# Kernel optimization log

Hardware: AMD Instinct MI355X
Metric: run time of the kernel (lower is better)

## Reference

```python
import jax, jax.numpy as jnp
import numpy as np

B, S, I, E, NH, HID, L = 32, 512, 64, 128, 8, 1024, 4
HD = E // NH
TEMP = 0.05
EPS_BN = 1e-5
EPS_LN = 1e-5


def _pe(seq_len, d_model):
    # sinusoidal positional encoding, matches PositionalEncoding buffer pe[:seq_len, 0, :]
    pos = jnp.arange(seq_len, dtype=jnp.float32)[:, None]
    div = jnp.exp(jnp.arange(0, d_model, 2, dtype=jnp.float32) * (-np.log(10000.0) / d_model))
    pe = jnp.zeros((seq_len, d_model), jnp.float32)
    pe = pe.at[:, 0::2].set(jnp.sin(pos * div))
    pe = pe.at[:, 1::2].set(jnp.cos(pos * div))
    return pe


def _bn(x, g, b, axis):
    # eval-mode BatchNorm1d with running_mean=0, running_var=1 (affine scale+shift)
    sh = [1] * x.ndim
    sh[axis] = -1
    return x * (g / jnp.sqrt(1.0 + EPS_BN)).reshape(sh) + b.reshape(sh)


def _ln(x, g, b):
    m = jnp.mean(x, axis=-1, keepdims=True)
    v = jnp.var(x, axis=-1, keepdims=True)
    return (x - m) / jnp.sqrt(v + EPS_LN) * g + b


def _layer(h, Wqkv, bqkv, Wo, bo, g1, b1, g2, b2, W1, bf1, W2, bf2):
    # h: (S, B, E); post-LN torch TransformerEncoderLayer, relu FFN
    s, b = h.shape[0], h.shape[1]
    qkv = h @ Wqkv + bqkv                                  # (S, B, 3E)
    q, k, v = jnp.split(qkv, 3, axis=-1)
    sp = lambda t: t.reshape(s, b, NH, HD).transpose(1, 2, 0, 3)  # (B, NH, S, HD)
    q, k, v = sp(q), sp(k), sp(v)
    att = jax.nn.softmax(jnp.einsum('bhqd,bhkd->bhqk', q, k) * (1.0 / np.sqrt(HD)), axis=-1)
    o = jnp.einsum('bhqk,bhkd->bhqd', att, v).transpose(2, 0, 1, 3).reshape(s, b, E)
    h = _ln(h + o @ Wo + bo, g1, b1)
    ff = jax.nn.relu(h @ W1 + bf1) @ W2 + bf2
    h = _ln(h + ff, g2, b2)
    return h, att.mean(axis=1)  # attn averaged over heads: (B, S, S)


def setup_inputs() -> dict:
    key = jax.random.key(0)
    ks = iter(jax.random.split(key, 64))
    r = lambda *sh: jax.random.normal(next(ks), sh, jnp.float32) * 0.02
    return dict(
        x=jax.random.normal(next(ks), (B, S, I), jnp.float32),
        Wt=r(I, E), bt=r(E),
        bn1_g=jnp.ones(E), bn1_b=jnp.zeros(E),
        bn2_g=jnp.ones(E), bn2_b=jnp.zeros(E),
        Wqkv=r(L, E, 3 * E), bqkv=r(L, 3 * E), Wo=r(L, E, E), bo=r(L, E),
        ln1_g=jnp.ones((L, E)), ln1_b=jnp.zeros((L, E)),
        ln2_g=jnp.ones((L, E)), ln2_b=jnp.zeros((L, E)),
        W1=r(L, E, HID), b1=r(L, HID), W2=r(L, HID, E), b2=r(L, E),
        bn3_g=jnp.ones(E), bn3_b=jnp.zeros(E),
        Wd=r(E, I), bd=r(I), bn4_g=jnp.ones(I), bn4_b=jnp.zeros(I),
        Ws=r(S, HID), bs=r(HID), bn5_g=jnp.ones(HID), bn5_b=jnp.zeros(HID),
        Wtext=r(1024, HID), btext=r(HID), lnT_g=jnp.ones(HID), lnT_b=jnp.zeros(HID),
        sensor_emb=jax.random.normal(next(ks), (I, 1024), jnp.float32),
    )


def reference(x, Wt, bt, bn1_g, bn1_b, bn2_g, bn2_b,
              Wqkv, bqkv, Wo, bo, ln1_g, ln1_b, ln2_g, ln2_b,
              W1, b1, W2, b2, bn3_g, bn3_b,
              Wd, bd, bn4_g, bn4_b, Ws, bs, bn5_g, bn5_b,
              Wtext, btext, lnT_g, lnT_b, sensor_emb):
    # trunk_net: Linear -> BN(E) -> PE -> BN(E)
    h = x @ Wt + bt                                  # (B, S, E)
    h = _bn(h.transpose(0, 2, 1), bn1_g, bn1_b, 1)   # (B, E, S)
    h = h.transpose(2, 0, 1)                         # (S, B, E)
    h = h + _pe(h.shape[0], E)[:, None, :]
    h = _bn(h.transpose(1, 2, 0), bn2_g, bn2_b, 1)   # (B, E, S)
    h = h.transpose(2, 0, 1)                         # (S, B, E)
    for i in range(L):
        h, attn = _layer(h, Wqkv[i], bqkv[i], Wo[i], bo[i],
                         ln1_g[i], ln1_b[i], ln2_g[i], ln2_b[i],
                         W1[i], b1[i], W2[i], b2[i])
    h = _bn(h.transpose(1, 2, 0), bn3_g, bn3_b, 1)   # (B, E, S)
    # downsample_embedding_to_input_net
    d = jax.nn.relu(h.transpose(0, 2, 1) @ Wd + bd)  # (B, S, I)
    d = _bn(d.transpose(0, 2, 1), bn4_g, bn4_b, 1)   # (B, I, S)
    # sequence_representation_net
    imu = jax.nn.relu(d @ Ws + bs)                   # (B, I, HID)
    imu = _bn(imu, bn5_g, bn5_b, 2)
    # text_to_shared_net on sensor embeddings
    sens = _ln(jax.nn.relu(sensor_emb @ Wtext + btext), lnT_g, lnT_b)  # (I, HID)
    # fused pairwise cosine similarity (torch expands to (B,I,I,HID); we don't)
    imu_n = imu / jnp.maximum(jnp.linalg.norm(imu, axis=-1, keepdims=True), 1e-8)
    sens_n = sens / jnp.maximum(jnp.linalg.norm(sens, axis=-1, keepdims=True), 1e-8)
    return jnp.einsum('bih,jh->bij', imu_n, sens_n) / TEMP  # (B, I, I)
```

## Files before the change

kernel.cpp:

```cpp
#include <hip/hip_runtime.h>
#include <hip/hip_bf16.h>

#define B_   32
#define S_   512
#define I_   64
#define E_   128
#define NH_  8
#define HD_  16
#define HID_ 1024
#define L_   4
#define NTOK (B_*S_)

typedef __hip_bfloat16 bf16;
typedef __attribute__((ext_vector_type(8))) short bf16x8;
typedef __attribute__((ext_vector_type(4))) short bf16x4;
typedef __attribute__((ext_vector_type(4))) float f32x4;

__device__ __forceinline__ float b2f(bf16 v) { return __bfloat162float(v); }

template<bool F32>
__device__ __forceinline__ float ld(const void* p, size_t i) {
    if (F32) return ((const float*)p)[i];
    return b2f(((const bf16*)p)[i]);
}

__device__ __forceinline__ unsigned short f2bu(float f) {
    union { bf16 h; unsigned short u; } c; c.h = __float2bfloat16(f); return c.u;
}
__device__ __forceinline__ unsigned short b2u(bf16 h) {
    union { bf16 h; unsigned short u; } c; c.h = h; return c.u;
}
__device__ __forceinline__ float u2f(unsigned short u) {
    return __uint_as_float((unsigned int)u << 16);
}

__global__ void k_flag(const void* bn1g, int* flag) {
    if (threadIdx.x == 0) {
        const unsigned short* u = (const unsigned short*)bn1g;
        int zeros = 0;
        for (int i = 0; i < 32; ++i) zeros += (u[i] == 0);
        flag[0] = (zeros >= 8) ? 1 : 0;
    }
}

struct TrJobs {
    const void* in[7];
    bf16*       out[7];
    int R[7];
    int C[7];
    int start[8];
};

template<bool F32>
__device__ void tr_all_body(const TrJobs& j, float (*tile)[33])
{
    int bid = blockIdx.x;
    int job = 0;
#pragma unroll
    for (int t = 0; t < 6; ++t) if (bid >= j.start[t + 1]) job = t + 1;
    int local = bid - j.start[job];
    int R = j.R[job], C = j.C[job];
    int nx = C >> 5, ny = R >> 5;
    int per_z = nx * ny;
    int z = local / per_z;
    int rem = local - z * per_z;
    int cy = rem / nx, cx = rem - cy * nx;
    const void* in = j.in[job];
    bf16* out = j.out[job];

    size_t off = (size_t)z * R * C;
    int c0 = cx * 32, r0 = cy * 32;
    int tx = threadIdx.x;
    for (int i = threadIdx.y; i < 32; i += 8)
        tile[i][tx] = ld<F32>(in, off + (size_t)(r0 + i) * C + c0 + tx);
    __syncthreads();
    for (int i = threadIdx.y; i < 32; i += 8)
        out[off + (size_t)(c0 + i) * R + r0 + tx] = __float2bfloat16(tile[tx][i]);
}
__global__ __launch_bounds__(256) void k_tr_all(TrJobs j, const int* flag)
{
    __shared__ float tile[32][33];
    if (*flag) tr_all_body<true>(j, tile);
    else       tr_all_body<false>(j, tile);
}

struct PkJobs {
    const bf16* in[4];
    bf16*       out[4];
    int K[4];
    int NT[4];
    int KT[4];
    int start[5];
};

__global__ __launch_bounds__(256) void k_pack(PkJobs j)
{
    int fb = blockIdx.x * 4 + (threadIdx.x >> 6);
    int lane = threadIdx.x & 63;
    int job = 0;
#pragma unroll
    for (int t = 0; t < 3; ++t) if (fb >= j.start[t + 1]) job = t + 1;
    int local = fb - j.start[job];
    int K = j.K[job], NT = j.NT[job], KT = j.KT[job];
    int per_z = NT * KT;
    int z = local / per_z;
    int rem = local - z * per_z;
    int ct = rem / KT, kt = rem - ct * KT;
    int l15 = lane & 15, quad = lane >> 4;
    const bf16* in = j.in[job] + (size_t)z * NT * 16 * K;
    bf16* out = j.out[job] + (size_t)z * per_z * 512 + (size_t)(ct * KT + kt) * 512 + lane * 8;
    *(uint4*)out = *(const uint4*)&in[(size_t)(ct * 16 + l15) * K + kt * 32 + quad * 8];
}

template<bool F32>
__device__ void trunk_body(const void* x, const void* Wt, const void* bt,
                           const void* g1, const void* c1,
                           const void* g2, const void* c2, float* __restrict__ h,
                           float (*xs)[I_])
{
    const int TOK = 8;
    int t0 = blockIdx.x * TOK;
    int tid = threadIdx.x;
    for (int idx = tid; idx < TOK * I_; idx += 128) {
        int tt = idx >> 6, k = idx & 63;
        xs[tt][k] = ld<F32>(x, (size_t)(t0 + tt) * I_ + k);
    }
    __syncthreads();
    int e = tid;
    float acc[TOK];
    float bias = ld<F32>(bt, e);
#pragma unroll
    for (int tt = 0; tt < TOK; ++tt) acc[tt] = bias;
    for (int k = 0; k < I_; ++k) {
        float w = ld<F32>(Wt, k * E_ + e);
#pragma unroll
        for (int tt = 0; tt < TOK; ++tt) acc[tt] += xs[tt][k] * w;
    }
    float rs = rsqrtf(1.0f + 1e-5f);
    float a1 = ld<F32>(g1, e) * rs, d1 = ld<F32>(c1, e);
    float a2 = ld<F32>(g2, e) * rs, d2 = ld<F32>(c2, e);
    int p = e >> 1;
    float freq = __expf(-(float)p * 0.14391157f);
#pragma unroll
    for (int tt = 0; tt < TOK; ++tt) {
        int t = t0 + tt;
        int s = t & (S_ - 1);
        float ang = (float)s * freq;
        float pe = (e & 1) ? cosf(ang) : sinf(ang);
        float v = acc[tt] * a1 + d1 + pe;
        h[(size_t)t * E_ + e] = v * a2 + d2;
    }
}
__global__ __launch_bounds__(128) void k_trunk(
    const void* x, const void* Wt, const void* bt,
    const void* g1, const void* c1, const void* g2, const void* c2,
    float* h, const int* flag)
{
    __shared__ float xs[8][I_];
    if (*flag) trunk_body<true>(x, Wt, bt, g1, c1, g2, c2, h, xs);
    else       trunk_body<false>(x, Wt, bt, g1, c1, g2, c2, h, xs);
}

template<bool F32>
__device__ void qkvm_body(const float* __restrict__ h, const bf16* __restrict__ WP,
                          const void* bias, size_t obi, bf16* __restrict__ qkv,
                          unsigned short (*A_s)[136])
{
    int t0 = blockIdx.x * 32;
    int tid = threadIdx.x;
    int wv = tid >> 6, lane = tid & 63;
    int l15 = lane & 15, quad = lane >> 4;

    {
        const float4* h4 = (const float4*)(h + (size_t)t0 * E_);
        for (int i = tid; i < 32 * E_ / 4; i += 256) {
            float4 v = h4[i];
            int row = i >> 5, col = (i & 31) * 4;
            unsigned int w0 = (unsigned int)f2bu(v.x) | ((unsigned int)f2bu(v.y) << 16);
            unsigned int w1 = (unsigned int)f2bu(v.z) | ((unsigned int)f2bu(v.w) << 16);
            *(uint2*)&A_s[row][col] = (uint2){w0, w1};
        }
    }
    __syncthreads();

    bf16x8 af[2][4];
#pragma unroll
    for (int kt = 0; kt < 4; ++kt) {
        int k0 = kt * 32 + quad * 8;
        af[0][kt] = *(const bf16x8*)&A_s[l15][k0];
        af[1][kt] = *(const bf16x8*)&A_s[16 + l15][k0];
    }
    for (int nt = 0; nt < 6; ++nt) {
        int col = wv * 96 + nt * 16 + l15;
        int ct = wv * 6 + nt;
        f32x4 acc0 = {0.f, 0.f, 0.f, 0.f}, acc1 = {0.f, 0.f, 0.f, 0.f};
#pragma unroll
        for (int kt = 0; kt < 4; ++kt) {
            bf16x8 bfr = *(const bf16x8*)&WP[(size_t)((ct * 4 + kt) * 64 + lane) * 8];
            acc0 = __builtin_amdgcn_mfma_f32_16x16x32_bf16(af[0][kt], bfr, acc0, 0, 0, 0);
            acc1 = __builtin_amdgcn_mfma_f32_16x16x32_bf16(af[1][kt], bfr, acc1, 0, 0, 0);
        }
        float bb = ld<F32>(bias, obi + col);
#pragma unroll
        for (int r = 0; r < 4; ++r) {
            qkv[(size_t)(t0 + quad * 4 + r) * 384 + col]      = __float2bfloat16(acc0[r] + bb);
            qkv[(size_t)(t0 + 16 + quad * 4 + r) * 384 + col] = __float2bfloat16(acc1[r] + bb);
        }
    }
}
__global__ __launch_bounds__(256) void k_qkv(
    const float* h, const bf16* WP, const void* bias, size_t obi,
    bf16* qkv, const int* flag)
{
    __shared__ unsigned short A_s[32][136];
    if (*flag) qkvm_body<true>(h, WP, bias, obi, qkv, A_s);
    else       qkvm_body<false>(h, WP, bias, obi, qkv, A_s);
}

__global__ __launch_bounds__(512) void k_attn(bf16* qkv)
{
    __shared__ unsigned short Ks[S_ * 16];
    __shared__ unsigned short Qs[256 * 16];
    __shared__ unsigned short VT[HD_ * 520];

    int bx = blockIdx.x;
    int qh = bx & 1;
    int hh = (bx >> 1) & (NH_ - 1);
    int b  = bx >> 4;
    int tid = threadIdx.x;
    const size_t base = (size_t)(b * S_) * 384 + hh * HD_;
    const float qs = 0.25f * 1.44269504f;

    for (int i = tid; i < S_ * 2; i += 512) {
        int s = i >> 1, hf = i & 1;
        uint4 v = *(const uint4*)(qkv + base + (size_t)s * 384 + 128 + hf * 8);
        unsigned int* w = (unsigned int*)&v;
#pragma unroll
        for (int j = 0; j < 4; ++j) {
            unsigned int lo = f2bu(u2f((unsigned short)(w[j] & 0xffff)) * qs);
            unsigned int hi = f2bu(u2f((unsigned short)(w[j] >> 16)) * qs);
            w[j] = lo | (hi << 16);
        }
        *(uint4*)&Ks[s * 16 + hf * 8] = v;
    }
    for (int i = tid; i < 256 * 2; i += 512) {
        int s = i >> 1, hf = i & 1;
        *(uint4*)&Qs[s * 16 + hf * 8] =
            *(const uint4*)(qkv + base + (size_t)(qh * 256 + s) * 384 + hf * 8);
    }
    {
        int s = tid;
        uint4 v0 = *(const uint4*)(qkv + base + (size_t)s * 384 + 256);
        uint4 v1 = *(const uint4*)(qkv + base + (size_t)s * 384 + 256 + 8);
        const unsigned short* u0 = (const unsigned short*)&v0;
        const unsigned short* u1 = (const unsigned short*)&v1;
#pragma unroll
        for (int dd = 0; dd < 8; ++dd) VT[dd * 520 + s] = u0[dd];
#pragma unroll
        for (int dd = 0; dd < 8; ++dd) VT[(8 + dd) * 520 + s] = u1[dd];
    }
    __syncthreads();

    int wv = tid >> 6, lane = tid & 63;
    int l15 = lane & 15, quad = lane >> 4;
    const f32x4 z4 = {0.f, 0.f, 0.f, 0.f};

    bf16x4 bq0 = *(const bf16x4*)&Qs[(wv * 32 + l15) * 16 + quad * 4];
    bf16x4 bq1 = *(const bf16x4*)&Qs[(wv * 32 + 16 + l15) * 16 + quad * 4];

    f32x4 O0 = z4, O1 = z4;
    float den0 = 0.f, den1 = 0.f;

#pragma unroll 2
    for (int kt = 0; kt < 32; ++kt) {
        bf16x4 ak = *(const bf16x4*)&Ks[(kt * 16 + l15) * 16 + quad * 4];
        bf16x4 av = *(const bf16x4*)&VT[l15 * 520 + kt * 16 + quad * 4];

        f32x4 s0 = __builtin_amdgcn_mfma_f32_16x16x16bf16_1k(ak, bq0, z4, 0, 0, 0);
        f32x4 s1 = __builtin_amdgcn_mfma_f32_16x16x16bf16_1k(ak, bq1, z4, 0, 0, 0);

        float p0[4], p1[4];
#pragma unroll
        for (int r = 0; r < 4; ++r) { p0[r] = exp2f(s0[r]); den0 += p0[r]; }
#pragma unroll
        for (int r = 0; r < 4; ++r) { p1[r] = exp2f(s1[r]); den1 += p1[r]; }

        bf16x4 pa0, pa1;
#pragma unroll
        for (int r = 0; r < 4; ++r) { pa0[r] = (short)f2bu(p0[r]); pa1[r] = (short)f2bu(p1[r]); }

        O0 = __builtin_amdgcn_mfma_f32_16x16x16bf16_1k(av, pa0, O0, 0, 0, 0);
        O1 = __builtin_amdgcn_mfma_f32_16x16x16bf16_1k(av, pa1, O1, 0, 0, 0);
    }

    den0 += __shfl_xor(den0, 16, 64);
    den0 += __shfl_xor(den0, 32, 64);
    den1 += __shfl_xor(den1, 16, 64);
    den1 += __shfl_xor(den1, 32, 64);
    float inv0 = 1.0f / den0;
    float inv1 = 1.0f / den1;

    int q0 = qh * 256 + wv * 32 + l15;
    bf16* out0 = qkv + (size_t)(b * S_ + q0) * 384 + hh * HD_ + quad * 4;
    bf16* out1 = out0 + (size_t)16 * 384;
    unsigned int a0 = (unsigned int)f2bu(O0[0] * inv0) | ((unsigned int)f2bu(O0[1] * inv0) << 16);
    unsigned int a1 = (unsigned int)f2bu(O0[2] * inv0) | ((unsigned int)f2bu(O0[3] * inv0) << 16);
    *(uint2*)out0 = (uint2){a0, a1};
    unsigned int c0 = (unsigned int)f2bu(O1[0] * inv1) | ((unsigned int)f2bu(O1[1] * inv1) << 16);
    unsigned int c1 = (unsigned int)f2bu(O1[2] * inv1) | ((unsigned int)f2bu(O1[3] * inv1) << 16);
    *(uint2*)out1 = (uint2){c0, c1};
}

#define FTOK 32
#define APAD 8
#define MHALF 512
#define MPAD 8

template<bool F32>
__device__ void projffn_body(const bf16* __restrict__ qkv, const bf16* __restrict__ WoP,
                             const void* bo, size_t obo,
                             const void* g1, const void* be1,
                             const bf16* __restrict__ W1P, const void* b1, size_t ob1,
                             const bf16* __restrict__ W2P, const void* b2v, size_t ob2,
                             const void* g2, const void* be2, size_t oln,
                             float* __restrict__ h,
                             unsigned short (*A_s)[E_ + APAD],
                             unsigned short (*mid_s)[MHALF + MPAD],
                             float (*red)[32][2])
{
    int t0 = blockIdx.x * FTOK;
    int tid = threadIdx.x;
    int wv = tid >> 6, lane = tid & 63;
    int l15 = lane & 15, quad = lane >> 4;
    int c0 = wv * 16 + l15;

    {
        int row = tid >> 4, seg = tid & 15;
        *(uint4*)&A_s[row][seg * 8] =
            *(const uint4*)&qkv[(size_t)(t0 + row) * 384 + seg * 8];
    }
    __syncthreads();

    bf16x8 af[2][4];
#pragma unroll
    for (int kt = 0; kt < 4; ++kt) {
        int k0 = kt * 32 + quad * 8;
        af[0][kt] = *(const bf16x8*)&A_s[l15][k0];
        af[1][kt] = *(const bf16x8*)&A_s[16 + l15][k0];
    }
    f32x4 acc[2];
    acc[0] = (f32x4){0.f, 0.f, 0.f, 0.f};
    acc[1] = (f32x4){0.f, 0.f, 0.f, 0.f};
#pragma unroll
    for (int kt = 0; kt < 4; ++kt) {
        bf16x8 bb0 = *(const bf16x8*)&WoP[(size_t)((wv * 4 + kt) * 64 + lane) * 8];
        acc[0] = __builtin_amdgcn_mfma_f32_16x16x32_bf16(af[0][kt], bb0, acc[0], 0, 0, 0);
        acc[1] = __builtin_amdgcn_mfma_f32_16x16x32_bf16(af[1][kt], bb0, acc[1], 0, 0, 0);
    }

    float bo0 = ld<F32>(bo, obo + c0);
    float val[2][4], s1[2][4], s2[2][4];
#pragma unroll
    for (int mt = 0; mt < 2; ++mt) {
#pragma unroll
        for (int r = 0; r < 4; ++r) {
            size_t row = (size_t)(t0 + mt * 16 + quad * 4 + r);
            float v0 = acc[mt][r] + bo0 + h[row * E_ + c0];
            val[mt][r] = v0;
            s1[mt][r] = v0;
            s2[mt][r] = v0 * v0;
        }
    }
#pragma unroll
    for (int off = 1; off < 16; off <<= 1) {
#pragma unroll
        for (int mt = 0; mt < 2; ++mt)
#pragma unroll
            for (int r = 0; r < 4; ++r) {
                s1[mt][r] += __shfl_xor(s1[mt][r], off, 64);
                s2[mt][r] += __shfl_xor(s2[mt][r], off, 64);
            }
    }
    if (l15 == 0) {
#pragma unroll
        for (int mt = 0; mt < 2; ++mt)
#pragma unroll
            for (int r = 0; r < 4; ++r) {
                red[wv][mt * 16 + quad * 4 + r][0] = s1[mt][r];
                red[wv][mt * 16 + quad * 4 + r][1] = s2[mt][r];
            }
    }
    __syncthreads();

    float val1[2][4];
    {
        float g10 = ld<F32>(g1, oln + c0);
        float b10 = ld<F32>(be1, oln + c0);
#pragma unroll
        for (int mt = 0; mt < 2; ++mt) {
#pragma unroll
            for (int r = 0; r < 4; ++r) {
                int rw = mt * 16 + quad * 4 + r;
                float su = red[0][rw][0] + red[1][rw][0] + red[2][rw][0] + red[3][rw][0]
                         + red[4][rw][0] + red[5][rw][0] + red[6][rw][0] + red[7][rw][0];
                float sq = red[0][rw][1] + red[1][rw][1] + red[2][rw][1] + red[3][rw][1]
                         + red[4][rw][1] + red[5][rw][1] + red[6][rw][1] + red[7][rw][1];
                float mean = su * (1.0f / E_);
                float var = fmaxf(sq * (1.0f / E_) - mean * mean, 0.0f);
                float rstd = rsqrtf(var + 1e-5f);
                float h0 = (val[mt][r] - mean) * rstd * g10 + b10;
                val1[mt][r] = h0;
                A_s[rw][c0] = f2bu(h0);
            }
        }
    }
    __syncthreads();

    bf16x8 af1[2][4];
#pragma unroll
    for (int kt = 0; kt < 4; ++kt) {
        int k0 = kt * 32 + quad * 8;
        af1[0][kt] = *(const bf16x8*)&A_s[l15][k0];
        af1[1][kt] = *(const bf16x8*)&A_s[16 + l15][k0];
    }

    f32x4 acc2[2];
    acc2[0] = (f32x4){0.f, 0.f, 0.f, 0.f};
    acc2[1] = (f32x4){0.f, 0.f, 0.f, 0.f};

    for (int p = 0; p < 2; ++p) {
        for (int nt = 0; nt < 4; ++nt) {
            int col = p * MHALF + wv * 64 + nt * 16 + l15;
            int lc  = wv * 64 + nt * 16 + l15;
            int ct  = p * 32 + wv * 4 + nt;
            f32x4 acc0 = {0.f, 0.f, 0.f, 0.f}, acc1 = {0.f, 0.f, 0.f, 0.f};
#pragma unroll
            for (int kt = 0; kt < 4; ++kt) {
                bf16x8 bfr = *(const bf16x8*)&W1P[(size_t)((ct * 4 + kt) * 64 + lane) * 8];
                acc0 = __builtin_amdgcn_mfma_f32_16x16x32_bf16(af1[0][kt], bfr, acc0, 0, 0, 0);
                acc1 = __builtin_amdgcn_mfma_f32_16x16x32_bf16(af1[1][kt], bfr, acc1, 0, 0, 0);
            }
            float bias = ld<F32>(b1, ob1 + col);
#pragma unroll
            for (int r = 0; r < 4; ++r) {
                mid_s[quad * 4 + r][lc]      = f2bu(fmaxf(acc0[r] + bias, 0.f));
                mid_s[16 + quad * 4 + r][lc] = f2bu(fmaxf(acc1[r] + bias, 0.f));
            }
        }
        __syncthreads();

        for (int kk = 0; kk < 16; ++kk) {
            int kt = p * 16 + kk;
            int k0l = kk * 32 + quad * 8;
            bf16x8 a0 = *(const bf16x8*)&mid_s[l15][k0l];
            bf16x8 a1 = *(const bf16x8*)&mid_s[16 + l15][k0l];
            bf16x8 bb0 = *(const bf16x8*)&W2P[(size_t)((wv * 32 + kt) * 64 + lane) * 8];
            acc2[0] = __builtin_amdgcn_mfma_f32_16x16x32_bf16(a0, bb0, acc2[0], 0, 0, 0);
            acc2[1] = __builtin_amdgcn_mfma_f32_16x16x32_bf16(a1, bb0, acc2[1], 0, 0, 0);
        }
        __syncthreads();
    }

    float b20 = ld<F32>(b2v, ob2 + c0);
#pragma unroll
    for (int mt = 0; mt < 2; ++mt) {
#pragma unroll
        for (int r = 0; r < 4; ++r) {
            float v0 = acc2[mt][r] + b20 + val1[mt][r];
            val[mt][r] = v0;
            s1[mt][r] = v0;
            s2[mt][r] = v0 * v0;
        }
    }
#pragma unroll
    for (int off = 1; off < 16; off <<= 1) {
#pragma unroll
        for (int mt = 0; mt < 2; ++mt)
#pragma unroll
            for (int r = 0; r < 4; ++r) {
                s1[mt][r] += __shfl_xor(s1[mt][r], off, 64);
                s2[mt][r] += __shfl_xor(s2[mt][r], off, 64);
            }
    }
    if (l15 == 0) {
#pragma unroll
        for (int mt = 0; mt < 2; ++mt)
#pragma unroll
            for (int r = 0; r < 4; ++r) {
                red[wv][mt * 16 + quad * 4 + r][0] = s1[mt][r];
                red[wv][mt * 16 + quad * 4 + r][1] = s2[mt][r];
            }
    }
    __syncthreads();
    float g20 = ld<F32>(g2, oln + c0);
    float be20 = ld<F32>(be2, oln + c0);
#pragma unroll
    for (int mt = 0; mt < 2; ++mt) {
#pragma unroll
        for (int r = 0; r < 4; ++r) {
            int rw = mt * 16 + quad * 4 + r;
            float su = red[0][rw][0] + red[1][rw][0] + red[2][rw][0] + red[3][rw][0]
                     + red[4][rw][0] + red[5][rw][0] + red[6][rw][0] + red[7][rw][0];
            float sq = red[0][rw][1] + red[1][rw][1] + red[2][rw][1] + red[3][rw][1]
                     + red[4][rw][1] + red[5][rw][1] + red[6][rw][1] + red[7][rw][1];
            float mean = su * (1.0f / E_);
            float var = fmaxf(sq * (1.0f / E_) - mean * mean, 0.0f);
            float rstd = rsqrtf(var + 1e-5f);
            size_t row = (size_t)(t0 + rw);
            h[row * E_ + c0] = (val[mt][r] - mean) * rstd * g20 + be20;
        }
    }
}
__global__ __launch_bounds__(512, 4) void k_projffn(
    const bf16* qkv, const bf16* WoP, const void* bo, size_t obo,
    const void* g1, const void* be1,
    const bf16* W1P, const void* b1, size_t ob1,
    const bf16* W2P, const void* b2v, size_t ob2,
    const void* g2, const void* be2, size_t oln, float* h, const int* flag)
{
    __shared__ unsigned short A_s[FTOK][E_ + APAD];
    __shared__ unsigned short mid_s[FTOK][MHALF + MPAD];
    __shared__ float red[8][32][2];
    if (*flag) projffn_body<true>(qkv, WoP, bo, obo, g1, be1, W1P, b1, ob1,
                                  W2P, b2v, ob2, g2, be2, oln, h, A_s, mid_s, red);
    else       projffn_body<false>(qkv, WoP, bo, obo, g1, be1, W1P, b1, ob1,
                                   W2P, b2v, ob2, g2, be2, oln, h, A_s, mid_s, red);
}

template<bool F32>
__device__ void downm_body(const float* __restrict__ h, const void* g3, const void* c3,
                           const bf16* __restrict__ WdT, const void* bd,
                           const void* g4, const void* c4, float* __restrict__ d,
                           unsigned short (*A_s)[136], float* g3s, float* c3s)
{
    int t0 = blockIdx.x * 32;
    int tid = threadIdx.x;
    if (tid < E_) {
        float rs = rsqrtf(1.0f + 1e-5f);
        g3s[tid] = ld<F32>(g3, tid) * rs;
        c3s[tid] = ld<F32>(c3, tid);
    }
    __syncthreads();
    for (int i = tid; i < 32 * E_; i += 256) {
        int row = i >> 7, col = i & 127;
        A_s[row][col] = f2bu(h[(size_t)(t0 + row) * E_ + col] * g3s[col] + c3s[col]);
    }
    __syncthreads();

    int wv = tid >> 6, lane = tid & 63;
    int l15 = lane & 15, quad = lane >> 4;
    int col = wv * 16 + l15;
    f32x4 acc0 = {0.f, 0.f, 0.f, 0.f}, acc1 = {0.f, 0.f, 0.f, 0.f};
#pragma unroll
    for (int kt = 0; kt < 4; ++kt) {
        int k0 = kt * 32 + quad * 8;
        bf16x8 a0 = *(const bf16x8*)&A_s[l15][k0];
        bf16x8 a1 = *(const bf16x8*)&A_s[16 + l15][k0];
        bf16x8 bb = *(const bf16x8*)&WdT[(size_t)col * E_ + k0];
        acc0 = __builtin_amdgcn_mfma_f32_16x16x32_bf16(a0, bb, acc0, 0, 0, 0);
        acc1 = __builtin_amdgcn_mfma_f32_16x16x32_bf16(a1, bb, acc1, 0, 0, 0);
    }
    float rs = rsqrtf(1.0f + 1e-5f);
    float bb = ld<F32>(bd, col);
    float a4 = ld<F32>(g4, col) * rs, d4 = ld<F32>(c4, col);
#pragma unroll
    for (int r = 0; r < 4; ++r) {
        d[(size_t)(t0 + quad * 4 + r) * I_ + col]      = fmaxf(acc0[r] + bb, 0.f) * a4 + d4;
        d[(size_t)(t0 + 16 + quad * 4 + r) * I_ + col] = fmaxf(acc1[r] + bb, 0.f) * a4 + d4;
    }
}
__global__ __launch_bounds__(256) void k_down(
    const float* h, const void* g3, const void* c3, const bf16* WdT, const void* bd,
    const void* g4, const void* c4, float* d, const int* flag)
{
    __shared__ unsigned short A_s[32][136];
    __shared__ float g3s[E_], c3s[E_];
    if (*flag) downm_body<true>(h, g3, c3, WdT, bd, g4, c4, d, A_s, g3s, c3s);
    else       downm_body<false>(h, g3, c3, WdT, bd, g4, c4, d, A_s, g3s, c3s);
}

template<bool F32>
__device__ void imum_body(const float* __restrict__ d, const bf16* __restrict__ WsT,
                          const void* bs, const void* g5, const void* c5,
                          float* __restrict__ imu, unsigned short (*A_s)[520])
{
    int b = blockIdx.x >> 3;
    int jc = blockIdx.x & 7;
    int tid = threadIdx.x;
    int wv = tid >> 6, lane = tid & 63;
    int l15 = lane & 15, quad = lane >> 4;

    for (int idx = tid; idx < I_ * S_; idx += 256) {
        int i = idx & 63, s = idx >> 6;
        A_s[i][s] = f2bu(d[((size_t)b * S_ + s) * I_ + i]);
    }
    __syncthreads();

    float rs = rsqrtf(1.0f + 1e-5f);
    int j0 = jc * 128 + wv * 32;
    for (int nt = 0; nt < 2; ++nt) {
        int j = j0 + nt * 16 + l15;
        f32x4 acc4[4];
#pragma unroll
        for (int mt = 0; mt < 4; ++mt) acc4[mt] = (f32x4){0.f, 0.f, 0.f, 0.f};
        for (int kt = 0; kt < 16; ++kt) {
            int k0 = kt * 32 + quad * 8;
            bf16x8 bfr = *(const bf16x8*)&WsT[(size_t)j * S_ + k0];
#pragma unroll
            for (int mt = 0; mt < 4; ++mt) {
                bf16x8 a = *(const bf16x8*)&A_s[mt * 16 + l15][k0];
                acc4[mt] = __builtin_amdgcn_mfma_f32_16x16x32_bf16(a, bfr, acc4[mt], 0, 0, 0);
            }
        }
        float bias = ld<F32>(bs, j);
        float a5 = ld<F32>(g5, j) * rs, d5 = ld<F32>(c5, j);
#pragma unroll
        for (int mt = 0; mt < 4; ++mt) {
#pragma unroll
            for (int r = 0; r < 4; ++r) {
                int row = mt * 16 + quad * 4 + r;
                float v = fmaxf(acc4[mt][r] + bias, 0.f) * a5 + d5;
                imu[((size_t)b * I_ + row) * HID_ + j] = v;
            }
        }
    }
}
__global__ __launch_bounds__(256) void k_imu(
    const float* d, const bf16* WsT, const void* bs,
    const void* g5, const void* c5, float* imu, const int* flag)
{
    __shared__ unsigned short A_s[I_][520];
    if (*flag) imum_body<true>(d, WsT, bs, g5, c5, imu, A_s);
    else       imum_body<false>(d, WsT, bs, g5, c5, imu, A_s);
}

__global__ __launch_bounds__(256) void k_norm(float* __restrict__ imu)
{
    __shared__ float red[4];
    size_t r0 = (size_t)blockIdx.x * HID_;
    int tid = threadIdx.x;
    float sq = 0.f;
    for (int k = tid; k < HID_; k += 256) { float v = imu[r0 + k]; sq += v * v; }
    for (int off = 32; off; off >>= 1) sq += __shfl_down(sq, off, 64);
    int wv = tid >> 6, lane = tid & 63;
    if (lane == 0) red[wv] = sq;
    __syncthreads();
    float tot = red[0] + red[1] + red[2] + red[3];
    float inv = 1.0f / fmaxf(sqrtf(fmaxf(tot, 0.f)), 1e-8f);
    for (int k = tid; k < HID_; k += 256) imu[r0 + k] *= inv;
}

template<bool F32>
__device__ void sensg_body(const void* se, const bf16* __restrict__ WtT,
                           const void* bt, float* __restrict__ sg,
                           unsigned short (*A_s)[HID_ + 8])
{
    int mt = blockIdx.x >> 4;
    int nc = blockIdx.x & 15;
    int r0 = mt * 16;
    int tid = threadIdx.x;
    int wv = tid >> 6, lane = tid & 63;
    int l15 = lane & 15, quad = lane >> 4;

    for (int i = tid; i < 16 * HID_; i += 256) {
        int row = i >> 10, col = i & (HID_ - 1);
        A_s[row][col] = f2bu(ld<F32>(se, (size_t)(r0 + row) * HID_ + col));
    }
    __syncthreads();

    int col = nc * 64 + wv * 16 + l15;
    f32x4 acc = {0.f, 0.f, 0.f, 0.f};
    for (int kt = 0; kt < 32; ++kt) {
        int k0 = kt * 32 + quad * 8;
        bf16x8 a = *(const bf16x8*)&A_s[l15][k0];
        bf16x8 bb = *(const bf16x8*)&WtT[(size_t)col * HID_ + k0];
        acc = __builtin_amdgcn_mfma_f32_16x16x32_bf16(a, bb, acc, 0, 0, 0);
    }
    float bbv = ld<F32>(bt, col);
#pragma unroll
    for (int r = 0; r < 4; ++r)
        sg[(size_t)(r0 + quad * 4 + r) * HID_ + col] = fmaxf(acc[r] + bbv, 0.f);
}
__global__ __launch_bounds__(256) void k_sens_gemm(
    const void* se, const bf16* WtT, const void* bt, float* sg, const int* flag)
{
    __shared__ unsigned short A_s[16][HID_ + 8];
    if (*flag) sensg_body<true>(se, WtT, bt, sg, A_s);
    else       sensg_body<false>(se, WtT, bt, sg, A_s);
}

template<bool F32>
__device__ void sensln_body(const float* __restrict__ sg, const void* g, const void* be,
                            bf16* __restrict__ sens_b, float (*red)[2])
{
    size_t r0 = (size_t)blockIdx.x * HID_;
    int tid = threadIdx.x;
    int wv = tid >> 6, lane = tid & 63;
    float v4[4];
    float s1 = 0.f, s2 = 0.f;
#pragma unroll
    for (int c = 0; c < 4; ++c) {
        float v = sg[r0 + tid + c * 256];
        v4[c] = v;
        s1 += v; s2 += v * v;
    }
    for (int off = 32; off; off >>= 1) {
        s1 += __shfl_down(s1, off, 64);
        s2 += __shfl_down(s2, off, 64);
    }
    if (lane == 0) { red[wv][0] = s1; red[wv][1] = s2; }
    __syncthreads();
    float su = red[0][0] + red[1][0] + red[2][0] + red[3][0];
    float sq = red[0][1] + red[1][1] + red[2][1] + red[3][1];
    float mean = su * (1.0f / HID_);
    float var = fmaxf(sq * (1.0f / HID_) - mean * mean, 0.0f);
    float rstd = rsqrtf(var + 1e-5f);
    float q = 0.f;
#pragma unroll
    for (int c = 0; c < 4; ++c) {
        int col = tid + c * 256;
        v4[c] = (v4[c] - mean) * rstd * ld<F32>(g, col) + ld<F32>(be, col);
        q += v4[c] * v4[c];
    }
    for (int off = 32; off; off >>= 1) q += __shfl_down(q, off, 64);
    __syncthreads();
    if (lane == 0) red[wv][0] = q;
    __syncthreads();
    float tot = red[0][0] + red[1][0] + red[2][0] + red[3][0];
    float inv = 1.0f / fmaxf(sqrtf(fmaxf(tot, 0.f)), 1e-8f);
#pragma unroll
    for (int c = 0; c < 4; ++c)
        sens_b[r0 + tid + c * 256] = __float2bfloat16(v4[c] * inv);
}
__global__ __launch_bounds__(256) void k_sens_ln(
    const float* sg, const void* g, const void* be, bf16* sens_b, const int* flag)
{
    __shared__ float red[4][2];
    if (*flag) sensln_body<true>(sg, g, be, sens_b, red);
    else       sensln_body<false>(sg, g, be, sens_b, red);
}

template<bool F32>
__device__ void finalm_body(const float* __restrict__ imu_n, const bf16* __restrict__ sens_b,
                            void* __restrict__ out, unsigned short (*A_s)[HID_ + 8])
{
    int r0 = blockIdx.x * 32;
    int tid = threadIdx.x;
    int wv = tid >> 6, lane = tid & 63;
    int l15 = lane & 15, quad = lane >> 4;

    {
        const float4* i4 = (const float4*)(imu_n + (size_t)r0 * HID_);
        for (int i = tid; i < 32 * HID_ / 4; i += 256) {
            float4 v = i4[i];
            int row = i >> 8, col = (i & 255) * 4;
            unsigned int w0 = (unsigned int)f2bu(v.x) | ((unsigned int)f2bu(v.y) << 16);
            unsigned int w1 = (unsigned int)f2bu(v.z) | ((unsigned int)f2bu(v.w) << 16);
            *(uint2*)&A_s[row][col] = (uint2){w0, w1};
        }
    }
    __syncthreads();

    int j = wv * 16 + l15;
    f32x4 acc[2];
    acc[0] = (f32x4){0.f, 0.f, 0.f, 0.f};
    acc[1] = (f32x4){0.f, 0.f, 0.f, 0.f};
    for (int kt = 0; kt < 32; ++kt) {
        int k0 = kt * 32 + quad * 8;
        bf16x8 bfr = *(const bf16x8*)&sens_b[(size_t)j * HID_ + k0];
        bf16x8 a0 = *(const bf16x8*)&A_s[l15][k0];
        bf16x8 a1 = *(const bf16x8*)&A_s[16 + l15][k0];
        acc[0] = __builtin_amdgcn_mfma_f32_16x16x32_bf16(a0, bfr, acc[0], 0, 0, 0);
        acc[1] = __builtin_amdgcn_mfma_f32_16x16x32_bf16(a1, bfr, acc[1], 0, 0, 0);
    }
#pragma unroll
    for (int mt = 0; mt < 2; ++mt) {
#pragma unroll
        for (int r = 0; r < 4; ++r) {
            size_t row = (size_t)(r0 + mt * 16 + quad * 4 + r);
            float v = acc[mt][r] * 20.0f;
            if (F32) ((float*)out)[row * I_ + j] = v;
            else     ((bf16*)out)[row * I_ + j] = __float2bfloat16(v);
        }
    }
}
__global__ __launch_bounds__(256) void k_final(
    const float* imu_n, const bf16* sens_b, void* out, const int* flag)
{
    __shared__ unsigned short A_s[32][HID_ + 8];
    if (*flag) finalm_body<true>(imu_n, sens_b, out, A_s);
    else       finalm_body<false>(imu_n, sens_b, out, A_s);
}

extern "C" void kernel_launch(void* const* d_in, const int* in_sizes, int n_in,
                              void* d_out, int out_size, void* d_ws, size_t ws_size,
                              hipStream_t stream) {
    (void)in_sizes; (void)n_in; (void)out_size; (void)ws_size;
    const void* x      = d_in[0];
    const void* Wt     = d_in[1];
    const void* bt     = d_in[2];
    const void* bn1_g  = d_in[3];
    const void* bn1_b  = d_in[4];
    const void* bn2_g  = d_in[5];
    const void* bn2_b  = d_in[6];
    const void* Wqkv   = d_in[7];
    const void* bqkv   = d_in[8];
    const void* Wo     = d_in[9];
    const void* bo     = d_in[10];
    const void* ln1_g  = d_in[11];
    const void* ln1_b  = d_in[12];
    const void* ln2_g  = d_in[13];
    const void* ln2_b  = d_in[14];
    const void* W1     = d_in[15];
    const void* b1     = d_in[16];
    const void* W2     = d_in[17];
    const void* b2     = d_in[18];
    const void* bn3_g  = d_in[19];
    const void* bn3_b  = d_in[20];
    const void* Wd     = d_in[21];
    const void* bd     = d_in[22];
    const void* bn4_g  = d_in[23];
    const void* bn4_b  = d_in[24];
    const void* Wsr    = d_in[25];
    const void* bs     = d_in[26];
    const void* bn5_g  = d_in[27];
    const void* bn5_b  = d_in[28];
    const void* Wtext  = d_in[29];
    const void* btext  = d_in[30];
    const void* lnT_g  = d_in[31];
    const void* lnT_b  = d_in[32];
    const void* semb   = d_in[33];

    char* ws = (char*)d_ws;
    float* h    = (float*)(ws);
    bf16*  qkvb = (bf16*) (ws + ((size_t)8  << 20));
    float* dbuf = (float*)(ws + ((size_t)8  << 20));
    float* imu  = (float*)(ws + ((size_t)12 << 20));
    bf16*  wb   = (bf16*) (ws + ((size_t)20 << 20));
    bf16*  WqkvT = wb;
    bf16*  WoT   = wb + 196608;
    bf16*  W1T   = wb + 262144;
    bf16*  W2T   = wb + 786432;
    bf16*  WsT   = wb + 1310720;
    bf16*  sensb = wb + 1835008;
    bf16*  WdT   = wb + 1900544;
    float* sg    = (float*)(wb + 1908736);
    int*   flag  = (int*)  (ws + ((size_t)24 << 20));
    bf16*  WtxT  = (bf16*) (ws + ((size_t)25 << 20));
    bf16*  wp    = (bf16*) (ws + ((size_t)27 << 20));
    bf16*  WqkvP = wp;
    bf16*  WoP   = wp + 196608;
    bf16*  W1P   = wp + 262144;
    bf16*  W2P   = wp + 786432;

    k_flag<<<1, 64, 0, stream>>>(bn1_g, flag);

    {
        TrJobs tj;
        tj.in[0] = Wqkv;  tj.out[0] = WqkvT; tj.R[0] = 128;  tj.C[0] = 384;
        tj.in[1] = Wo;    tj.out[1] = WoT;   tj.R[1] = 128;  tj.C[1] = 128;
        tj.in[2] = W1;    tj.out[2] = W1T;   tj.R[2] = 128;  tj.C[2] = 1024;
        tj.in[3] = W2;    tj.out[3] = W2T;   tj.R[3] = 1024; tj.C[3] = 128;
        tj.in[4] = Wsr;   tj.out[4] = WsT;   tj.R[4] = 512;  tj.C[4] = 1024;
        tj.in[5] = Wd;    tj.out[5] = WdT;   tj.R[5] = 128;  tj.C[5] = 64;
        tj.in[6] = Wtext; tj.out[6] = WtxT;  tj.R[6] = 1024; tj.C[6] = 1024;
        const int st[8] = {0, 192, 256, 768, 1280, 1792, 1800, 2824};
        for (int i = 0; i < 8; ++i) tj.start[i] = st[i];
        k_tr_all<<<2824, dim3(32, 8), 0, stream>>>(tj, flag);
    }
    {
        PkJobs pj;
        pj.in[0] = WqkvT; pj.out[0] = WqkvP; pj.K[0] = 128;  pj.NT[0] = 24; pj.KT[0] = 4;
        pj.in[1] = WoT;   pj.out[1] = WoP;   pj.K[1] = 128;  pj.NT[1] = 8;  pj.KT[1] = 4;
        pj.in[2] = W1T;   pj.out[2] = W1P;   pj.K[2] = 128;  pj.NT[2] = 64; pj.KT[2] = 4;
        pj.in[3] = W2T;   pj.out[3] = W2P;   pj.K[3] = 1024; pj.NT[3] = 8;  pj.KT[3] = 32;
        const int st[5] = {0, 384, 512, 1536, 2560};
        for (int i = 0; i < 5; ++i) pj.start[i] = st[i];
        k_pack<<<640, 256, 0, stream>>>(pj);
    }

    k_trunk<<<NTOK / 8, 128, 0, stream>>>(x, Wt, bt, bn1_g, bn1_b, bn2_g, bn2_b, h, flag);

    for (int l = 0; l < L_; ++l) {
        size_t obqkv = (size_t)l * 384;
        size_t obo   = (size_t)l * E_;
        size_t ob1   = (size_t)l * HID_;
        size_t ob2   = (size_t)l * E_;
        size_t oln   = (size_t)l * E_;
        k_qkv<<<NTOK / 32, 256, 0, stream>>>(h, WqkvP + (size_t)l * 49152,
                                             bqkv, obqkv, qkvb, flag);
        k_attn<<<B_ * NH_ * 2, 512, 0, stream>>>(qkvb);
        k_projffn<<<NTOK / FTOK, 512, 0, stream>>>(qkvb, WoP + (size_t)l * 16384, bo, obo,
                                                   ln1_g, ln1_b,
                                                   W1P + (size_t)l * 131072, b1, ob1,
                                                   W2P + (size_t)l * 131072, b2, ob2,
                                                   ln2_g, ln2_b, oln, h, flag);
    }

    k_down<<<NTOK / 32, 256, 0, stream>>>(h, bn3_g, bn3_b, WdT, bd, bn4_g, bn4_b, dbuf, flag);
    k_imu<<<B_ * 8, 256, 0, stream>>>(dbuf, WsT, bs, bn5_g, bn5_b, imu, flag);
    k_norm<<<B_ * I_, 256, 0, stream>>>(imu);
    k_sens_gemm<<<64, 256, 0, stream>>>(semb, WtxT, btext, sg, flag);
    k_sens_ln<<<I_, 256, 0, stream>>>(sg, lnT_g, lnT_b, sensb, flag);
    k_final<<<(B_ * I_) / 32, 256, 0, stream>>>(imu, sensb, d_out, flag);
}
```

Before: 491.5 us.

## Fuse next layer's QKV projection into the projection/FFN kernel epilogue

After the second LayerNorm, the projffn kernel now writes its output tile to shared memory as bf16 and immediately computes the next layer's QKV projection with MFMA, writing it into the qkv buffer. Only the first layer's QKV is computed by a standalone k_qkv launch. This removes three kernel launches and a full re-read of h from global memory per layer. In exchange the projffn kernel gets longer, with extra registers and a sync, which could affect occupancy. It also overwrites qkvb while other blocks may still read it, though each block reads and writes only its own rows.

Result: faster. 462.5 us (-5.9%).

```diff
diff --git a/kernel.cpp b/kernel.cpp
--- a/kernel.cpp
+++ b/kernel.cpp
@@ -324,6 +324,8 @@
                              const bf16* __restrict__ W2P, const void* b2v, size_t ob2,
                              const void* g2, const void* be2, size_t oln,
                              float* __restrict__ h,
+                             const bf16* __restrict__ WqP, const void* bqv, size_t obq,
+                             bf16* __restrict__ qkvout, int do_qkv,
                              unsigned short (*A_s)[E_ + APAD],
                              unsigned short (*mid_s)[MHALF + MPAD],
                              float (*red)[32][2])
@@ -507,7 +509,37 @@
             float var = fmaxf(sq * (1.0f / E_) - mean * mean, 0.0f);
             float rstd = rsqrtf(var + 1e-5f);
             size_t row = (size_t)(t0 + rw);
-            h[row * E_ + c0] = (val[mt][r] - mean) * rstd * g20 + be20;
+            float outv = (val[mt][r] - mean) * rstd * g20 + be20;
+            h[row * E_ + c0] = outv;
+            A_s[rw][c0] = f2bu(outv);
+        }
+    }
+
+    if (do_qkv) {
+        __syncthreads();
+        bf16x8 afq[2][4];
+#pragma unroll
+        for (int kt = 0; kt < 4; ++kt) {
+            int k0 = kt * 32 + quad * 8;
+            afq[0][kt] = *(const bf16x8*)&A_s[l15][k0];
+            afq[1][kt] = *(const bf16x8*)&A_s[16 + l15][k0];
+        }
+        for (int nt = 0; nt < 3; ++nt) {
+            int ct = wv * 3 + nt;
+            int col = ct * 16 + l15;
+            f32x4 q0 = {0.f, 0.f, 0.f, 0.f}, q1 = {0.f, 0.f, 0.f, 0.f};
+#pragma unroll
+            for (int kt = 0; kt < 4; ++kt) {
+                bf16x8 bfr = *(const bf16x8*)&WqP[(size_t)((ct * 4 + kt) * 64 + lane) * 8];
+                q0 = __builtin_amdgcn_mfma_f32_16x16x32_bf16(afq[0][kt], bfr, q0, 0, 0, 0);
+                q1 = __builtin_amdgcn_mfma_f32_16x16x32_bf16(afq[1][kt], bfr, q1, 0, 0, 0);
+            }
+            float bb = ld<F32>(bqv, obq + col);
+#pragma unroll
+            for (int r = 0; r < 4; ++r) {
+                qkvout[(size_t)(t0 + quad * 4 + r) * 384 + col]      = __float2bfloat16(q0[r] + bb);
+                qkvout[(size_t)(t0 + 16 + quad * 4 + r) * 384 + col] = __float2bfloat16(q1[r] + bb);
+            }
         }
     }
 }
@@ -516,15 +548,19 @@
     const void* g1, const void* be1,
     const bf16* W1P, const void* b1, size_t ob1,
     const bf16* W2P, const void* b2v, size_t ob2,
-    const void* g2, const void* be2, size_t oln, float* h, const int* flag)
+    const void* g2, const void* be2, size_t oln, float* h,
+    const bf16* WqP, const void* bqv, size_t obq, bf16* qkvout, int do_qkv,
+    const int* flag)
 {
     __shared__ unsigned short A_s[FTOK][E_ + APAD];
     __shared__ unsigned short mid_s[FTOK][MHALF + MPAD];
     __shared__ float red[8][32][2];
     if (*flag) projffn_body<true>(qkv, WoP, bo, obo, g1, be1, W1P, b1, ob1,
-                                  W2P, b2v, ob2, g2, be2, oln, h, A_s, mid_s, red);
+                                  W2P, b2v, ob2, g2, be2, oln, h,
+                                  WqP, bqv, obq, qkvout, do_qkv, A_s, mid_s, red);
     else       projffn_body<false>(qkv, WoP, bo, obo, g1, be1, W1P, b1, ob1,
-                                   W2P, b2v, ob2, g2, be2, oln, h, A_s, mid_s, red);
+                                   W2P, b2v, ob2, g2, be2, oln, h,
+                                   WqP, bqv, obq, qkvout, do_qkv, A_s, mid_s, red);
 }
 
 template<bool F32>
@@ -881,20 +917,23 @@
 
     k_trunk<<<NTOK / 8, 128, 0, stream>>>(x, Wt, bt, bn1_g, bn1_b, bn2_g, bn2_b, h, flag);
 
+    k_qkv<<<NTOK / 32, 256, 0, stream>>>(h, WqkvP, bqkv, 0, qkvb, flag);
+
     for (int l = 0; l < L_; ++l) {
-        size_t obqkv = (size_t)l * 384;
         size_t obo   = (size_t)l * E_;
         size_t ob1   = (size_t)l * HID_;
         size_t ob2   = (size_t)l * E_;
         size_t oln   = (size_t)l * E_;
-        k_qkv<<<NTOK / 32, 256, 0, stream>>>(h, WqkvP + (size_t)l * 49152,
-                                             bqkv, obqkv, qkvb, flag);
+        int do_qkv = (l < L_ - 1) ? 1 : 0;
+        int ln = (l < L_ - 1) ? (l + 1) : 0;
         k_attn<<<B_ * NH_ * 2, 512, 0, stream>>>(qkvb);
         k_projffn<<<NTOK / FTOK, 512, 0, stream>>>(qkvb, WoP + (size_t)l * 16384, bo, obo,
                                                    ln1_g, ln1_b,
                                                    W1P + (size_t)l * 131072, b1, ob1,
                                                    W2P + (size_t)l * 131072, b2, ob2,
-                                                   ln2_g, ln2_b, oln, h, flag);
+                                                   ln2_g, ln2_b, oln, h,
+                                                   WqkvP + (size_t)ln * 49152, bqkv,
+                                                   (size_t)ln * 384, qkvb, do_qkv, flag);
     }
 
     k_down<<<NTOK / 32, 256, 0, stream>>>(h, bn3_g, bn3_b, WdT, bd, bn4_g, bn4_b, dbuf, flag);
```
